# Kernel optimization log

Hardware: AMD Instinct MI355X
Metric: run time of the kernel (lower is better)

Reference implementation:

```python
import jax, jax.numpy as jnp
import numpy as np
import math

N, L, S, H, E, D = 2, 2048, 2048, 16, 64, 64

def setup_inputs() -> dict:
    key = jax.random.key(0)
    kq, kk, kv = jax.random.split(key, 3)
    return {
        "queries": jax.random.normal(kq, (N, L, H, E), dtype=jnp.float32),
        "keys": jax.random.normal(kk, (N, S, H, E), dtype=jnp.float32),
        "values": jax.random.normal(kv, (N, S, H, D), dtype=jnp.float32),
        "attn_mask": jnp.zeros((L, S), dtype=jnp.float32),  # additive mask
    }

def reference(queries, keys, values, attn_mask):
    e = queries.shape[-1]
    softmax_temp = 1.0 / math.sqrt(e)  # self.softmax_temp is None -> 1/sqrt(E)
    # (N,L,H,E) x (N,S,H,E) -> (N,H,L,S)
    qk = jnp.einsum('nlhe,nshe->nhls', queries, keys)
    qk = qk + attn_mask  # additive mask broadcast over (N,H)
    att = jax.nn.softmax(softmax_temp * qk, axis=-1)
    # dropout rate 0.0 (eval) -> identity
    v = jnp.einsum('nhls,nshd->nlhd', att, values)
    return v
```

## Files before the change

### kernel.cpp

```cpp
#include <hip/hip_runtime.h>
#include <hip/hip_bf16.h>


typedef short bf16x8 __attribute__((ext_vector_type(8)));
typedef short short4v __attribute__((ext_vector_type(4)));
typedef unsigned uint2v __attribute__((ext_vector_type(2)));
typedef unsigned uint4v __attribute__((ext_vector_type(4)));
typedef float f32x4 __attribute__((ext_vector_type(4)));

constexpr int Nb = 2, Lq = 2048, Sk = 2048, Hh = 16, Ee = 64, Dd = 64;
constexpr int BM = 128;
constexpr int BN = 64;
constexpr int NT = Sk / BN;
constexpr int KVB = 4096;
constexpr int MSKB = 2048;
constexpr float SCALE_LOG2E = 0.125f * 1.4426950408889634f;

__device__ __forceinline__ short f2bf(float f) {
  union { float f; unsigned u; } v; v.f = f;
  unsigned r = (v.u + 0x7fffu + ((v.u >> 16) & 1u)) >> 16;
  return (short)r;
}

__device__ __forceinline__ unsigned pack_bf16x2(float a, float b) {
  union { __hip_bfloat162 h; unsigned u; } v;
  float2 f; f.x = a; f.y = b;
  v.h = __float22bfloat162_rn(f);
  return v.u;
}

__device__ __forceinline__ float bf_lo(unsigned u) { return __uint_as_float(u << 16); }
__device__ __forceinline__ float bf_hi(unsigned u) { return __uint_as_float(u & 0xffff0000u); }

__device__ __forceinline__ void async_copy16(const void* g, void* l) {
  __builtin_amdgcn_global_load_lds(
      (const __attribute__((address_space(1))) unsigned int*)g,
      (__attribute__((address_space(3))) unsigned int*)l, 16, 0, 0);
}

__global__ __launch_bounds__(256) void prep_all(const float* __restrict__ K,
                                                const float* __restrict__ V,
                                                const float* __restrict__ M,
                                                short* __restrict__ KVf,
                                                short* __restrict__ Mg) {
  if (blockIdx.x < KVB) {
    int gid = blockIdx.x * 256 + threadIdx.x;
    int off8 = gid & 1023;
    int t  = (gid >> 10) & 31;
    int nh = gid >> 15;
    int n = nh >> 4, h = nh & 15;
    short* dst = KVf + ((size_t)(nh * NT + t)) * 8192 + off8 * 8;
    if (off8 < 512) {
      int ch = off8 >> 6;
      int l  = off8 & 63;
      int sb = ch >> 1, kc = ch & 1, c = l & 15, quad = l >> 4;
      const float* p = K + (((size_t)n * Sk + (t * 64 + sb * 16 + c)) * Hh + h) * Ee
                         + kc * 32 + quad * 8;
      float4 x = *(const float4*)(p);
      float4 y = *(const float4*)(p + 4);
      bf16x8 o;
      o[0] = f2bf(x.x); o[1] = f2bf(x.y); o[2] = f2bf(x.z); o[3] = f2bf(x.w);
      o[4] = f2bf(y.x); o[5] = f2bf(y.y); o[6] = f2bf(y.z); o[7] = f2bf(y.w);
      *(bf16x8*)dst = o;
    } else {
      int pos = off8 - 512;
      int vch = pos >> 5;
      int l0  = (pos & 31) * 2;
      int db = vch >> 2, sb = vch & 3;
      bf16x8 o;
#pragma unroll
      for (int i = 0; i < 2; ++i) {
        int l = l0 + i, c = l & 15, quad = l >> 4;
        const float* p = V + (((size_t)n * Sk + (t * 64 + sb * 16 + quad * 4)) * Hh + h) * Dd
                           + db * 16 + c;
#pragma unroll
        for (int j = 0; j < 4; ++j) o[i * 4 + j] = f2bf(p[(size_t)j * Hh * Dd]);
      }
      *(bf16x8*)dst = o;
    }
  } else {
    int u = (blockIdx.x - KVB) * 256 + threadIdx.x;
    int sub  = u & 3;
    int lane = (u >> 2) & 63;
    int t    = (u >> 8) & 31;
    int qw   = u >> 13;
    int cb = sub >> 1, sbp = sub & 1;
    int c = lane & 15, quad = lane >> 4;
    int row = (qw >> 2) * 128 + (qw & 3) * 32 + cb * 16 + c;
    short o[8];
#pragma unroll
    for (int k = 0; k < 2; ++k) {
      int sb = sbp * 2 + k;
      float4 mv = *(const float4*)(M + (size_t)row * Sk + t * 64 + sb * 16 + quad * 4);
      o[k * 4 + 0] = f2bf(mv.x * SCALE_LOG2E);
      o[k * 4 + 1] = f2bf(mv.y * SCALE_LOG2E);
      o[k * 4 + 2] = f2bf(mv.z * SCALE_LOG2E);
      o[k * 4 + 3] = f2bf(mv.w * SCALE_LOG2E);
    }
    *(bf16x8*)(Mg + (size_t)u * 8) = *(const bf16x8*)o;
  }
}

template <int NS>
__global__ __launch_bounds__(256, 4) void attn_fwd(
    const float* __restrict__ Q, const short* __restrict__ KVf,
    const short* __restrict__ Mg, float* __restrict__ P0,
    float* __restrict__ P1, float* __restrict__ rsW)
{
  __shared__ short KV[2][8192];

  const int tid  = threadIdx.x;
  const int lane = tid & 63;
  const int w    = tid >> 6;
  const int quad = lane >> 4;
  const int c    = lane & 15;

  const int id   = blockIdx.x;
  const int slot = id >> 3;
  const int nh   = (id & 7) * 4 + (slot & 3);
  const int qt   = (slot >> 2) & 15;
  const int sp   = (NS == 2) ? (slot >> 6) : 0;
  const int n    = nh >> 4;
  const int h    = nh & 15;

  const int row0 = qt * BM + w * 32;
  const int t0 = sp * (NT / NS), tc = NT / NS;

  bf16x8 qfrag[2][2];
#pragma unroll
  for (int cb = 0; cb < 2; ++cb) {
    const float* qp = Q + (((size_t)n * Lq + (row0 + cb * 16 + c)) * Hh + h) * Ee;
#pragma unroll
    for (int kc = 0; kc < 2; ++kc) {
      const float* p = qp + kc * 32 + quad * 8;
      float4 x = *(const float4*)(p);
      float4 y = *(const float4*)(p + 4);
      bf16x8 f;
      f[0] = f2bf(x.x * SCALE_LOG2E); f[1] = f2bf(x.y * SCALE_LOG2E);
      f[2] = f2bf(x.z * SCALE_LOG2E); f[3] = f2bf(x.w * SCALE_LOG2E);
      f[4] = f2bf(y.x * SCALE_LOG2E); f[5] = f2bf(y.y * SCALE_LOG2E);
      f[6] = f2bf(y.z * SCALE_LOG2E); f[7] = f2bf(y.w * SCALE_LOG2E);
      qfrag[cb][kc] = f;
    }
  }

  f32x4 o[2][4];
#pragma unroll
  for (int cb = 0; cb < 2; ++cb)
#pragma unroll
    for (int db = 0; db < 4; ++db) { o[cb][db][0] = 0.f; o[cb][db][1] = 0.f; o[cb][db][2] = 0.f; o[cb][db][3] = 0.f; }
  float rs[2] = {0.f, 0.f};

  const short* kvt = KVf + (size_t)nh * NT * 8192;
  const short* mbase = Mg + (size_t)(qt * 4 + w) * 65536 + lane * 32;

#pragma unroll
  for (int i = 0; i < 4; ++i) {
    int seg = w * 4 + i;
    async_copy16(kvt + ((size_t)t0 * 8192) + seg * 512 + lane * 8, &KV[0][seg * 512 + lane * 8]);
  }
  uint4v mcur[4], mnxt[4];
#pragma unroll
  for (int i = 0; i < 4; ++i) mcur[i] = *(const uint4v*)(mbase + (size_t)t0 * 2048 + i * 8);
  __syncthreads();

  for (int tt = 0; tt < tc; ++tt) {
    const int t = t0 + tt;
    const int buf = tt & 1;

    if (tt + 1 < tc) {
      const short* gm = mbase + (size_t)(t + 1) * 2048;
#pragma unroll
      for (int i = 0; i < 4; ++i) mnxt[i] = *(const uint4v*)(gm + i * 8);
      const short* gk = kvt + (size_t)(t + 1) * 8192;
#pragma unroll
      for (int i = 0; i < 4; ++i) {
        int seg = w * 4 + i;
        async_copy16(gk + seg * 512 + lane * 8, &KV[buf ^ 1][seg * 512 + lane * 8]);
      }
    }

    const short* kb = &KV[buf][0];

    f32x4 sacc[2][4];
#pragma unroll
    for (int cb = 0; cb < 2; ++cb)
#pragma unroll
      for (int sbp = 0; sbp < 2; ++sbp) {
        uint4v m = mcur[cb * 2 + sbp];
        sacc[cb][sbp * 2 + 0][0] = bf_lo(m.x); sacc[cb][sbp * 2 + 0][1] = bf_hi(m.x);
        sacc[cb][sbp * 2 + 0][2] = bf_lo(m.y); sacc[cb][sbp * 2 + 0][3] = bf_hi(m.y);
        sacc[cb][sbp * 2 + 1][0] = bf_lo(m.z); sacc[cb][sbp * 2 + 1][1] = bf_hi(m.z);
        sacc[cb][sbp * 2 + 1][2] = bf_lo(m.w); sacc[cb][sbp * 2 + 1][3] = bf_hi(m.w);
      }

#pragma unroll
    for (int kc = 0; kc < 2; ++kc) {
#pragma unroll
      for (int sb = 0; sb < 4; ++sb) {
        bf16x8 kfrag = *(const bf16x8*)&kb[(sb * 2 + kc) * 512 + lane * 8];
#pragma unroll
        for (int cb = 0; cb < 2; ++cb)
          sacc[cb][sb] = __builtin_amdgcn_mfma_f32_16x16x32_bf16(kfrag, qfrag[cb][kc], sacc[cb][sb], 0, 0, 0);
      }
    }

    short4v pv[2][4];
#pragma unroll
    for (int cb = 0; cb < 2; ++cb)
#pragma unroll
      for (int sb = 0; sb < 4; ++sb) {
        float p0 = __builtin_amdgcn_exp2f(sacc[cb][sb][0]);
        float p1 = __builtin_amdgcn_exp2f(sacc[cb][sb][1]);
        float p2 = __builtin_amdgcn_exp2f(sacc[cb][sb][2]);
        float p3 = __builtin_amdgcn_exp2f(sacc[cb][sb][3]);
        rs[cb] += (p0 + p1) + (p2 + p3);
        union { uint2v u; short4v s; } uu;
        uu.u.x = pack_bf16x2(p0, p1);
        uu.u.y = pack_bf16x2(p2, p3);
        pv[cb][sb] = uu.s;
      }

#pragma unroll
    for (int sb = 0; sb < 4; ++sb) {
#pragma unroll
      for (int db = 0; db < 4; ++db) {
        short4v vfrag = *(const short4v*)&kb[4096 + (db * 4 + sb) * 256 + lane * 4];
#pragma unroll
        for (int cb = 0; cb < 2; ++cb)
          o[cb][db] = __builtin_amdgcn_mfma_f32_16x16x16bf16_1k(vfrag, pv[cb][sb], o[cb][db], 0, 0, 0);
      }
    }

    __syncthreads();
#pragma unroll
    for (int i = 0; i < 4; ++i) mcur[i] = mnxt[i];
  }

  float* P = (sp == 0) ? P0 : P1;
#pragma unroll
  for (int cb = 0; cb < 2; ++cb) {
    float v = rs[cb];
    v += __shfl_xor(v, 16, 64);
    v += __shfl_xor(v, 32, 64);
    const int qrow = row0 + cb * 16 + c;
    if (quad == 0) rsW[(size_t)sp * 65536 + nh * 2048 + qrow] = v;
    float* op = P + (((size_t)n * Lq + qrow) * Hh + h) * Dd + quad * 4;
#pragma unroll
    for (int db = 0; db < 4; ++db) {
      float4 ov;
      ov.x = o[cb][db][0]; ov.y = o[cb][db][1];
      ov.z = o[cb][db][2]; ov.w = o[cb][db][3];
      *(float4*)(op + db * 16) = ov;
    }
  }
}

template <int NS>
__global__ __launch_bounds__(256) void combine(float* __restrict__ Out,
                                               const float* __restrict__ P1,
                                               const float* __restrict__ rsW) {
  int gid = blockIdx.x * 256 + threadIdx.x;
  size_t i4 = (size_t)gid * 4;
  int hh = (int)((i4 >> 6) & 15);
  int l  = (int)((i4 >> 10) & 2047);
  int nn = (int)(i4 >> 21);
  int nh = nn * 16 + hh;
  float rs = rsW[nh * 2048 + l];
  float4 v = *(const float4*)(Out + i4);
  if (NS == 2) {
    rs += rsW[65536 + (size_t)nh * 2048 + l];
    float4 b = *(const float4*)(P1 + i4);
    v.x += b.x; v.y += b.y; v.z += b.z; v.w += b.w;
  }
  float inv = 1.0f / rs;
  v.x *= inv; v.y *= inv; v.z *= inv; v.w *= inv;
  *(float4*)(Out + i4) = v;
}

extern "C" void kernel_launch(void* const* d_in, const int* in_sizes, int n_in,
                              void* d_out, int out_size, void* d_ws, size_t ws_size,
                              hipStream_t stream) {
  const float* Q   = (const float*)d_in[0];
  const float* K   = (const float*)d_in[1];
  const float* V   = (const float*)d_in[2];
  const float* Msk = (const float*)d_in[3];
  float* Out = (float*)d_out;

  short* KVf = (short*)d_ws;
  short* Mg  = KVf + (size_t)8388608;
  float* rsW = (float*)(Mg + (size_t)4194304);
  float* P1  = rsW + 131072;

  const size_t need2 = 16777216u + 8388608u + 524288u + 16777216u;
  const bool split = ws_size >= need2;

  prep_all<<<dim3(KVB + MSKB), dim3(256), 0, stream>>>(K, V, Msk, KVf, Mg);

  if (split) {
    attn_fwd<2><<<dim3(1024), dim3(256), 0, stream>>>(Q, KVf, Mg, Out, P1, rsW);
    combine<2><<<dim3(4096), dim3(256), 0, stream>>>(Out, P1, rsW);
  } else {
    attn_fwd<1><<<dim3(512), dim3(256), 0, stream>>>(Q, KVf, Mg, Out, P1, rsW);
    combine<1><<<dim3(4096), dim3(256), 0, stream>>>(Out, P1, rsW);
  }
}
```

Before: 166.3 us.

## Fuse split-K combine into attention kernel via atomic flag handoff

Removes the separate combine kernel. The two key-range halves of each query tile now coordinate through a per-slice atomic counter. The first block to finish writes its partial output in bf16 plus its row sums, and the second block spin-waits on the flag, then adds, normalizes and writes the final output. Row sums are now computed by an extra MFMA against a ones vector instead of scalar adds. This saves a kernel launch and a full fp32 partial round-trip, but it risks spin-wait stalls if partner blocks are not co-resident and adds precision loss from the bf16 partials.

```diff
diff --git a/kernel.cpp b/kernel.cpp
--- a/kernel.cpp
+++ b/kernel.cpp
@@ -42,7 +42,12 @@
                                                 const float* __restrict__ V,
                                                 const float* __restrict__ M,
                                                 short* __restrict__ KVf,
-                                                short* __restrict__ Mg) {
+                                                short* __restrict__ Mg,
+                                                int* __restrict__ Fl) {
+  if (blockIdx.x == 0) {
+    Fl[threadIdx.x] = 0;
+    Fl[threadIdx.x + 256] = 0;
+  }
   if (blockIdx.x < KVB) {
     int gid = blockIdx.x * 256 + threadIdx.x;
     int off8 = gid & 1023;
@@ -85,8 +90,8 @@
     int t    = (u >> 8) & 31;
     int qw   = u >> 13;
     int cb = sub >> 1, sbp = sub & 1;
-    int c = lane & 15, quad = lane >> 4;
-    int row = (qw >> 2) * 128 + (qw & 3) * 32 + cb * 16 + c;
+    int cc = lane & 15, quad = lane >> 4;
+    int row = (qw >> 2) * 128 + (qw & 3) * 32 + cb * 16 + cc;
     short o[8];
 #pragma unroll
     for (int k = 0; k < 2; ++k) {
@@ -101,13 +106,13 @@
   }
 }
 
-template <int NS>
 __global__ __launch_bounds__(256, 4) void attn_fwd(
     const float* __restrict__ Q, const short* __restrict__ KVf,
-    const short* __restrict__ Mg, float* __restrict__ P0,
-    float* __restrict__ P1, float* __restrict__ rsW)
+    const short* __restrict__ Mg, float* __restrict__ Out,
+    short* __restrict__ Pp, float* __restrict__ rsP, int* __restrict__ Fl)
 {
   __shared__ short KV[2][8192];
+  __shared__ int role;
 
   const int tid  = threadIdx.x;
   const int lane = tid & 63;
@@ -119,12 +124,12 @@
   const int slot = id >> 3;
   const int nh   = (id & 7) * 4 + (slot & 3);
   const int qt   = (slot >> 2) & 15;
-  const int sp   = (NS == 2) ? (slot >> 6) : 0;
+  const int sp   = slot >> 6;
   const int n    = nh >> 4;
   const int h    = nh & 15;
 
   const int row0 = qt * BM + w * 32;
-  const int t0 = sp * (NT / NS), tc = NT / NS;
+  const int t0 = sp * (NT / 2), tc = NT / 2;
 
   bf16x8 qfrag[2][2];
 #pragma unroll
@@ -144,12 +149,19 @@
     }
   }
 
-  f32x4 o[2][4];
-#pragma unroll
-  for (int cb = 0; cb < 2; ++cb)
+  short4v ones;
+  {
+    short one = (c == 0) ? (short)0x3F80 : (short)0;
+    ones[0] = one; ones[1] = one; ones[2] = one; ones[3] = one;
+  }
+
+  f32x4 o[2][4], o_rs[2];
+#pragma unroll
+  for (int cb = 0; cb < 2; ++cb) {
+    o_rs[cb][0] = 0.f; o_rs[cb][1] = 0.f; o_rs[cb][2] = 0.f; o_rs[cb][3] = 0.f;
 #pragma unroll
     for (int db = 0; db < 4; ++db) { o[cb][db][0] = 0.f; o[cb][db][1] = 0.f; o[cb][db][2] = 0.f; o[cb][db][3] = 0.f; }
-  float rs[2] = {0.f, 0.f};
+  }
 
   const short* kvt = KVf + (size_t)nh * NT * 8192;
   const short* mbase = Mg + (size_t)(qt * 4 + w) * 65536 + lane * 32;
@@ -214,7 +226,6 @@
         float p1 = __builtin_amdgcn_exp2f(sacc[cb][sb][1]);
         float p2 = __builtin_amdgcn_exp2f(sacc[cb][sb][2]);
         float p3 = __builtin_amdgcn_exp2f(sacc[cb][sb][3]);
-        rs[cb] += (p0 + p1) + (p2 + p3);
         union { uint2v u; short4v s; } uu;
         uu.u.x = pack_bf16x2(p0, p1);
         uu.u.y = pack_bf16x2(p2, p3);
@@ -230,6 +241,9 @@
         for (int cb = 0; cb < 2; ++cb)
           o[cb][db] = __builtin_amdgcn_mfma_f32_16x16x16bf16_1k(vfrag, pv[cb][sb], o[cb][db], 0, 0, 0);
       }
+#pragma unroll
+      for (int cb = 0; cb < 2; ++cb)
+        o_rs[cb] = __builtin_amdgcn_mfma_f32_16x16x16bf16_1k(ones, pv[cb][sb], o_rs[cb], 0, 0, 0);
     }
 
     __syncthreads();
@@ -237,45 +251,59 @@
     for (int i = 0; i < 4; ++i) mcur[i] = mnxt[i];
   }
 
-  float* P = (sp == 0) ? P0 : P1;
+  float rsv[2];
 #pragma unroll
   for (int cb = 0; cb < 2; ++cb) {
-    float v = rs[cb];
+    float v = o_rs[cb][0];
     v += __shfl_xor(v, 16, 64);
     v += __shfl_xor(v, 32, 64);
-    const int qrow = row0 + cb * 16 + c;
-    if (quad == 0) rsW[(size_t)sp * 65536 + nh * 2048 + qrow] = v;
-    float* op = P + (((size_t)n * Lq + qrow) * Hh + h) * Dd + quad * 4;
-#pragma unroll
-    for (int db = 0; db < 4; ++db) {
-      float4 ov;
-      ov.x = o[cb][db][0]; ov.y = o[cb][db][1];
-      ov.z = o[cb][db][2]; ov.w = o[cb][db][3];
-      *(float4*)(op + db * 16) = ov;
-    }
-  }
-}
-
-template <int NS>
-__global__ __launch_bounds__(256) void combine(float* __restrict__ Out,
-                                               const float* __restrict__ P1,
-                                               const float* __restrict__ rsW) {
-  int gid = blockIdx.x * 256 + threadIdx.x;
-  size_t i4 = (size_t)gid * 4;
-  int hh = (int)((i4 >> 6) & 15);
-  int l  = (int)((i4 >> 10) & 2047);
-  int nn = (int)(i4 >> 21);
-  int nh = nn * 16 + hh;
-  float rs = rsW[nh * 2048 + l];
-  float4 v = *(const float4*)(Out + i4);
-  if (NS == 2) {
-    rs += rsW[65536 + (size_t)nh * 2048 + l];
-    float4 b = *(const float4*)(P1 + i4);
-    v.x += b.x; v.y += b.y; v.z += b.z; v.w += b.w;
-  }
-  float inv = 1.0f / rs;
-  v.x *= inv; v.y *= inv; v.z *= inv; v.w *= inv;
-  *(float4*)(Out + i4) = v;
+    rsv[cb] = v;
+  }
+
+  const int slice = nh * 16 + qt;
+  if (tid == 0) role = atomicAdd(&Fl[slice], 1);
+  __syncthreads();
+
+  if (role == 0) {
+#pragma unroll
+    for (int cb = 0; cb < 2; ++cb) {
+      short* pp = Pp + ((size_t)(slice * 4 + w) * 2 + cb) * 1024 + lane * 4;
+#pragma unroll
+      for (int db = 0; db < 4; ++db) {
+        uint2v u;
+        u.x = pack_bf16x2(o[cb][db][0], o[cb][db][1]);
+        u.y = pack_bf16x2(o[cb][db][2], o[cb][db][3]);
+        *(uint2v*)(pp + db * 256) = u;
+      }
+      if (quad == 0) rsP[slice * 128 + w * 32 + cb * 16 + c] = rsv[cb];
+    }
+    __threadfence();
+    if (tid == 0) atomicAdd(&Fl[slice], 1);
+  } else {
+    if (tid == 0) {
+      while (atomicAdd(&Fl[slice], 0) < 3) __builtin_amdgcn_s_sleep(8);
+    }
+    __syncthreads();
+    __threadfence();
+#pragma unroll
+    for (int cb = 0; cb < 2; ++cb) {
+      const short* pp = Pp + ((size_t)(slice * 4 + w) * 2 + cb) * 1024 + lane * 4;
+      float rs_tot = rsv[cb] + rsP[slice * 128 + w * 32 + cb * 16 + c];
+      float inv = 1.0f / rs_tot;
+      const int qrow = row0 + cb * 16 + c;
+      float* op = Out + (((size_t)n * Lq + qrow) * Hh + h) * Dd + quad * 4;
+#pragma unroll
+      for (int db = 0; db < 4; ++db) {
+        uint2v u = *(const uint2v*)(pp + db * 256);
+        float4 ov;
+        ov.x = (o[cb][db][0] + bf_lo(u.x)) * inv;
+        ov.y = (o[cb][db][1] + bf_hi(u.x)) * inv;
+        ov.z = (o[cb][db][2] + bf_lo(u.y)) * inv;
+        ov.w = (o[cb][db][3] + bf_hi(u.y)) * inv;
+        *(float4*)(op + db * 16) = ov;
+      }
+    }
+  }
 }
 
 extern "C" void kernel_launch(void* const* d_in, const int* in_sizes, int n_in,
@@ -289,19 +317,10 @@
 
   short* KVf = (short*)d_ws;
   short* Mg  = KVf + (size_t)8388608;
-  float* rsW = (float*)(Mg + (size_t)4194304);
-  float* P1  = rsW + 131072;
-
-  const size_t need2 = 16777216u + 8388608u + 524288u + 16777216u;
-  const bool split = ws_size >= need2;
-
-  prep_all<<<dim3(KVB + MSKB), dim3(256), 0, stream>>>(K, V, Msk, KVf, Mg);
-
-  if (split) {
-    attn_fwd<2><<<dim3(1024), dim3(256), 0, stream>>>(Q, KVf, Mg, Out, P1, rsW);
-    combine<2><<<dim3(4096), dim3(256), 0, stream>>>(Out, P1, rsW);
-  } else {
-    attn_fwd<1><<<dim3(512), dim3(256), 0, stream>>>(Q, KVf, Mg, Out, P1, rsW);
-    combine<1><<<dim3(4096), dim3(256), 0, stream>>>(Out, P1, rsW);
-  }
-}
+  short* Pp  = Mg  + (size_t)4194304;
+  float* rsP = (float*)(Pp + (size_t)4194304);
+  int*   Fl  = (int*)(rsP + 65536);
+
+  prep_all<<<dim3(KVB + MSKB), dim3(256), 0, stream>>>(K, V, Msk, KVf, Mg, Fl);
+  attn_fwd<<<dim3(1024), dim3(256), 0, stream>>>(Q, KVf, Mg, Out, Pp, rsP, Fl);
+}
```

Result: slower. 240.1 us (+44.3%).
